# Kernel tuning notes

Hardware: AMD Instinct MI355X
Metric: run time of the kernel (lower is better)

The kernel has to match this reference:

```python
import jax, jax.numpy as jnp
import numpy as np

EMBED = 768
HEADS = 12
HEAD = EMBED // HEADS  # 64
NO_ROPE = 1
GRID = 32
S_IMG = GRID * GRID
SEQ = S_IMG + NO_ROPE
BATCH = 8
SCALE = HEAD ** -0.5


def _rope_tables():
    # VisionRotaryEmbeddingFast(dim=half_head_dim=HEAD//2, pt_seq_len=GRID)
    dim = HEAD // 2  # 32 per spatial axis
    inv_freq = 1.0 / (10000.0 ** (np.arange(0, dim, 2, dtype=np.float32) / dim))  # [dim//2]
    t = np.arange(GRID, dtype=np.float32)
    f = t[:, None] * inv_freq[None, :]              # [GRID, dim//2]
    f = np.repeat(f, 2, axis=-1)                    # interleaved pairs -> [GRID, dim]
    fh = np.broadcast_to(f[:, None, :], (GRID, GRID, dim))
    fw = np.broadcast_to(f[None, :, :], (GRID, GRID, dim))
    freqs = np.concatenate([fh, fw], axis=-1).reshape(S_IMG, HEAD)  # [S_IMG, HEAD]
    return jnp.asarray(np.cos(freqs)), jnp.asarray(np.sin(freqs))

ROPE_COS, ROPE_SIN = _rope_tables()


def _rel_pos_index():
    ch, cw = np.meshgrid(np.arange(GRID), np.arange(GRID), indexing='ij')
    coords = np.stack([ch.ravel(), cw.ravel()])          # [2, S_IMG]
    rel = coords[:, :, None] - coords[:, None, :]        # [2, S_IMG, S_IMG]
    rel = rel.transpose(1, 2, 0).astype(np.int64)
    rel[:, :, 0] += GRID - 1
    rel[:, :, 1] += GRID - 1
    rel[:, :, 0] *= 2 * GRID - 1
    return jnp.asarray(rel.sum(-1))                      # [S_IMG, S_IMG]

REL_INDEX = _rel_pos_index()


def _rotate_half(x):
    # pairs are interleaved: (d r) with r=2
    x2 = x.reshape(*x.shape[:-1], -1, 2)
    return jnp.stack([-x2[..., 1], x2[..., 0]], axis=-1).reshape(x.shape)


def _apply_rope(t):
    # t: [B, H, S, HEAD]; first NO_ROPE tokens bypass rope
    t_cls, t_img = t[:, :, :NO_ROPE, :], t[:, :, NO_ROPE:, :]
    t_img = t_img * ROPE_COS + _rotate_half(t_img) * ROPE_SIN
    return jnp.concatenate([t_cls, t_img], axis=2)


def setup_inputs() -> dict:
    key = jax.random.key(0)
    ks = jax.random.split(key, 6)
    std = EMBED ** -0.5
    return {
        'x': jax.random.normal(ks[0], (BATCH, SEQ, EMBED), jnp.float32),
        'qkv_w': jax.random.normal(ks[1], (3 * EMBED, EMBED), jnp.float32) * std,
        'qkv_b': jnp.zeros((3 * EMBED,), jnp.float32),
        'proj_w': jax.random.normal(ks[2], (EMBED, EMBED), jnp.float32) * std,
        'proj_b': jnp.zeros((EMBED,), jnp.float32),
        'rel_bias_table': jax.random.normal(ks[3], ((2 * GRID - 1) * (2 * GRID - 1), HEADS), jnp.float32) * 0.02,
        'key_padding_mask': jnp.zeros((BATCH, SEQ), jnp.bool_),
    }


def reference(x, qkv_w, qkv_b, proj_w, proj_b, rel_bias_table, key_padding_mask):
    B, S, _ = x.shape
    qkv = x @ qkv_w.T + qkv_b                                  # [B,S,3E]
    qkv = qkv.reshape(B, S, 3, HEADS, HEAD).transpose(2, 0, 3, 1, 4)
    q, k, v = qkv[0], qkv[1], qkv[2]                            # [B,H,S,D]
    q = _apply_rope(q)
    k = _apply_rope(k)
    scores = jnp.einsum('bhqd,bhkd->bhqk', q, k) * SCALE        # [B,H,S,S]
    # relative position bias on image-token sub-block
    bias = rel_bias_table[REL_INDEX]                            # [S_IMG,S_IMG,H]
    bias = bias.transpose(2, 0, 1)                              # [H,S_IMG,S_IMG]
    scores = scores.at[:, :, NO_ROPE:, NO_ROPE:].add(bias[None])
    neg = jnp.finfo(scores.dtype).min
    scores = jnp.where(key_padding_mask[:, None, None, :], neg, scores)
    attn = jax.nn.softmax(scores, axis=-1)
    ctx = jnp.einsum('bhqk,bhkd->bhqd', attn, v)
    ctx = ctx.transpose(0, 2, 1, 3).reshape(B, S, EMBED)
    return ctx @ proj_w.T + proj_b
```

## Files before the change

kernel.cpp:

```cpp
#include <hip/hip_runtime.h>
#include <math.h>

#define EMBED 768
#define NHEADS 12
#define HDIM 64
#define SEQ 1025
#define NBATCH 8
#define BHCOUNT (NBATCH*NHEADS)
#define MROWS (NBATCH*SEQ)
#define QKV_N (3*EMBED)
#define QKV_ELEMS (BHCOUNT*SEQ*HDIM)
#define BT_N 3969
#define MASKPAD 1088
#define QMUL 0.1803368801111204f
#define LOG2E 1.4426950408889634f
#define NX4 1574400
#define NW4 442368
#define NP4 147456

typedef __attribute__((ext_vector_type(8))) short bf16x8;
typedef __attribute__((ext_vector_type(4))) float f32x4;

static __device__ inline unsigned short f2bf(float f) {
    unsigned u = __float_as_uint(f);
    unsigned r = (u + 0x7FFF + ((u >> 16) & 1)) >> 16;
    return (unsigned short)r;
}

static __device__ inline unsigned int cvtpk(float a, float b) {
    unsigned int r;
    asm("v_cvt_pk_bf16_f32 %0, %1, %2" : "=v"(r) : "v"(a), "v"(b));
    return r;
}

static __device__ inline void gld16(const unsigned short* g, unsigned short* l) {
    __builtin_amdgcn_global_load_lds(
        (const __attribute__((address_space(1))) unsigned int*)g,
        (__attribute__((address_space(3))) unsigned int*)l,
        16, 0, 0);
}

__global__ __launch_bounds__(256)
void f2bf3_kernel(const float* __restrict__ x, const float* __restrict__ w,
                  const float* __restrict__ pw,
                  unsigned short* __restrict__ xbf, unsigned short* __restrict__ wbf,
                  unsigned short* __restrict__ pwbf)
{
    int i = blockIdx.x * 256 + threadIdx.x;
    const float* src; unsigned short* dst; int off;
    if (i < NX4)            { src = x;  dst = xbf;  off = i; }
    else if (i < NX4 + NW4) { src = w;  dst = wbf;  off = i - NX4; }
    else if (i < NX4 + NW4 + NP4) { src = pw; dst = pwbf; off = i - NX4 - NW4; }
    else return;
    float4 v = *reinterpret_cast<const float4*>(&src[off << 2]);
    ushort4 o;
    o.x = f2bf(v.x); o.y = f2bf(v.y); o.z = f2bf(v.z); o.w = f2bf(v.w);
    *reinterpret_cast<ushort4*>(&dst[off << 2]) = o;
}

__global__ __launch_bounds__(256)
void setup_tables_kernel(const float* __restrict__ bt, float* __restrict__ btT,
                         const unsigned char* __restrict__ m, unsigned char* __restrict__ mp,
                         float* __restrict__ cosT, float* __restrict__ sinT)
{
    const int bid = blockIdx.x, tid = threadIdx.x;
    if (bid < 256) {
        int s = (bid << 2) + (tid >> 6);
        int d = tid & 63;
        int pos = (d < 32) ? (s >> 5) : (s & 31);
        int j = (d & 31) >> 1;
        float ang = (float)pos * expf(-(float)j * 0.5756462732485115f);
        cosT[(s << 6) + d] = cosf(ang);
        sinT[(s << 6) + d] = sinf(ang);
    } else if (bid < 256 + 187) {
        int e = (bid - 256) * 256 + tid;
        if (e < NHEADS * BT_N) {
            int h = e / BT_N, idx = e - h * BT_N;
            btT[h * BT_N + idx] = bt[idx * NHEADS + h] * LOG2E;
        }
    } else {
        int b = bid - 443;
        for (int i = tid; i < MASKPAD; i += 256)
            mp[b * MASKPAD + i] = (i < SEQ) ? m[b * SEQ + i] : (unsigned char)0;
    }
}

__global__ __launch_bounds__(256)
void qkv_mfma_kernel(const unsigned short* __restrict__ xbf,
                     const unsigned short* __restrict__ wbf,
                     const float* __restrict__ bias,
                     const float* __restrict__ cosT, const float* __restrict__ sinT,
                     unsigned short* __restrict__ qout, unsigned short* __restrict__ kout,
                     unsigned short* __restrict__ vout)
{
    __shared__ unsigned short As[128][32];
    __shared__ unsigned short Bs[128][32];
    const int m0 = blockIdx.x * 128;
    const int n0 = blockIdx.y * 128;
    const int tid = threadIdx.x;
    const int w = tid >> 6, lane = tid & 63;
    const int li = lane & 15, lg = lane >> 4;
    const int wr = w >> 1, wc = w & 1;

    f32x4 acc[4][4];
    #pragma unroll
    for (int mi = 0; mi < 4; ++mi)
        #pragma unroll
        for (int nj = 0; nj < 4; ++nj) acc[mi][nj] = (f32x4){0.f, 0.f, 0.f, 0.f};

    for (int kt = 0; kt < 24; ++kt) {
        const int k0 = kt << 5;
        #pragma unroll
        for (int c = 0; c < 2; ++c) {
            const int idx = c * 256 + tid;
            const int row = idx >> 2, slot = idx & 3;
            int grow = m0 + row; if (grow > MROWS - 1) grow = MROWS - 1;
            gld16(&xbf[(long)grow * EMBED + k0 + slot * 8], &As[0][0] + idx * 8);
            gld16(&wbf[(long)(n0 + row) * EMBED + k0 + slot * 8], &Bs[0][0] + idx * 8);
        }
        __syncthreads();

        bf16x8 af[4], bfr[4];
        #pragma unroll
        for (int mi = 0; mi < 4; ++mi)
            af[mi] = *reinterpret_cast<const bf16x8*>(&As[wr * 64 + mi * 16 + li][lg * 8]);
        #pragma unroll
        for (int nj = 0; nj < 4; ++nj)
            bfr[nj] = *reinterpret_cast<const bf16x8*>(&Bs[wc * 64 + nj * 16 + li][lg * 8]);
        __builtin_amdgcn_s_setprio(1);
        #pragma unroll
        for (int mi = 0; mi < 4; ++mi)
            #pragma unroll
            for (int nj = 0; nj < 4; ++nj)
                acc[mi][nj] = __builtin_amdgcn_mfma_f32_16x16x32_bf16(
                    af[mi], bfr[nj], acc[mi][nj], 0, 0, 0);
        __builtin_amdgcn_s_setprio(0);
        __syncthreads();
    }

    int brow[4][4], srow[4][4];
    #pragma unroll
    for (int mi = 0; mi < 4; ++mi)
        #pragma unroll
        for (int r = 0; r < 4; ++r) {
            int m = m0 + wr * 64 + mi * 16 + lg * 4 + r;
            int mm = (m < MROWS) ? m : (MROWS - 1);
            int bb = mm / SEQ;
            brow[mi][r] = bb;
            srow[mi][r] = mm - bb * SEQ;
        }

    #pragma unroll
    for (int nj = 0; nj < 4; ++nj) {
        const int n = n0 + wc * 64 + nj * 16 + li;
        const int which = n / EMBED;
        const int nh = n - which * EMBED;
        const int h = nh >> 6, d = nh & 63;
        unsigned short* outp = (which == 0) ? qout : (which == 1) ? kout : vout;
        const float mul = (which == 0) ? QMUL : 1.0f;
        const float bn = bias[n];
        const bool dorope = which < 2;
        const float sgn = (d & 1) ? 1.f : -1.f;
        #pragma unroll
        for (int mi = 0; mi < 4; ++mi)
            #pragma unroll
            for (int r = 0; r < 4; ++r) {
                const int m = m0 + wr * 64 + mi * 16 + lg * 4 + r;
                float v = acc[mi][nj][r] + bn;
                float pv = __shfl_xor(v, 1, 64);
                if (m < MROWS) {
                    const int bb = brow[mi][r], s = srow[mi][r];
                    if (dorope && s >= 1) {
                        const int p = s - 1;
                        v = v * cosT[(p << 6) + d] + sgn * pv * sinT[(p << 6) + d];
                    }
                    outp[((long)(bb * NHEADS + h) * SEQ + s) * HDIM + d] = f2bf(v * mul);
                }
            }
    }
}

__global__ __launch_bounds__(256)
void attn_mfma_kernel(const unsigned short* __restrict__ qg,
                      const unsigned short* __restrict__ kg,
                      const unsigned short* __restrict__ vg,
                      const float* __restrict__ btT,
                      const unsigned char* __restrict__ maskpad,
                      unsigned short* __restrict__ ctx)
{
    __shared__ unsigned short QPs[64][64];
    __shared__ unsigned short Ks[2][64][64];
    __shared__ unsigned short Vts[2][64][64];

    const int i = (int)blockIdx.x;
    const int xcd = i & 7, jb = i >> 3;
    const int bh = xcd * 12 + (jb % 12);
    const int q0 = (jb / 12) * 64;
    const int b = bh / NHEADS, h = bh % NHEADS;
    const int tid = threadIdx.x;
    const int w = tid >> 6;
    const int lane = tid & 63;
    const int lg = lane >> 4;
    const int li = lane & 15;
    const int qrow = (w << 4) + li;
    const int swzr = (li & 7) << 3;

    const unsigned short* qbase = qg + (long)bh * (SEQ * HDIM);
    const unsigned short* kbase = kg + (long)bh * (SEQ * HDIM);
    const unsigned short* vbase = vg + (long)bh * (SEQ * HDIM);
    const unsigned char* maskp = maskpad + b * MASKPAD;
    const float* btTh = btT + h * BT_N;

    const int sidx0 = tid, sidx1 = 256 + tid;
    const int sr0 = sidx0 >> 3, sc0 = (sidx0 & 7) << 3;
    const int sr1 = sidx1 >> 3, sc1 = (sidx1 & 7) << 3;

    {
        int qi0 = q0 + sr0; if (qi0 > SEQ - 1) qi0 = SEQ - 1;
        int qi1 = q0 + sr1; if (qi1 > SEQ - 1) qi1 = SEQ - 1;
        gld16(&qbase[(long)qi0 * HDIM + (sc0 ^ ((sr0 & 7) << 3))], &QPs[0][0] + sidx0 * 8);
        gld16(&qbase[(long)qi1 * HDIM + (sc1 ^ ((sr1 & 7) << 3))], &QPs[0][0] + sidx1 * 8);
        gld16(&kbase[(long)sr0 * HDIM + (sc0 ^ ((sr0 & 7) << 3))], &Ks[0][0][0] + sidx0 * 8);
        gld16(&kbase[(long)sr1 * HDIM + (sc1 ^ ((sr1 & 7) << 3))], &Ks[0][0][0] + sidx1 * 8);
    }
    int4 vreg[2];
    vreg[0] = *reinterpret_cast<const int4*>(&vbase[(long)sr0 * HDIM + sc0]);
    vreg[1] = *reinterpret_cast<const int4*>(&vbase[(long)sr1 * HDIM + sc1]);
    __syncthreads();

    bf16x8 qf[2];
    #pragma unroll
    for (int dk = 0; dk < 2; ++dk)
        qf[dk] = *reinterpret_cast<const bf16x8*>(&QPs[qrow][(dk * 32 + (lg << 3)) ^ swzr]);

    const int qi_l = q0 + qrow;
    const float bq = (qi_l >= 1) ? 1.0f : 0.0f;
    int qp = qi_l - 1; if (qp < 0) qp = 0; if (qp > 1023) qp = 1023;
    const int qcode = (qp >> 5) * 63 + (qp & 31) + 1984;

    {
        union { int4 v; unsigned short u[8]; } t0, t1;
        t0.v = vreg[0]; t1.v = vreg[1];
        const int cb30 = sc0 >> 3, cb31 = sc1 >> 3;
        #pragma unroll
        for (int e = 0; e < 8; ++e) {
            Vts[0][sc0 + e][sr0 ^ (((e ^ cb30) & 7) << 3)] = t0.u[e];
            Vts[0][sc1 + e][sr1 ^ (((e ^ cb31) & 7) << 3)] = t1.u[e];
        }
    }
    __syncthreads();

    float m_l = -1e30f, l_l = 0.f;
    f32x4 acco[4];
    #pragma unroll
    for (int j = 0; j < 4; ++j) acco[j] = (f32x4){0.f, 0.f, 0.f, 0.f};

    int kc[4][4];
    for (int kt = 0; kt < 17; ++kt) {
        const int k0 = kt * 64;
        const int cur = kt & 1;

        if (kt < 16) {
            const int k0n = k0 + 64;
            vreg[0] = (k0n + sr0 < SEQ)
                ? *reinterpret_cast<const int4*>(&vbase[(long)(k0n + sr0) * HDIM + sc0])
                : make_int4(0, 0, 0, 0);
            vreg[1] = (k0n + sr1 < SEQ)
                ? *reinterpret_cast<const int4*>(&vbase[(long)(k0n + sr1) * HDIM + sc1])
                : make_int4(0, 0, 0, 0);
            int ki0 = k0n + sr0; if (ki0 > SEQ - 1) ki0 = SEQ - 1;
            int ki1 = k0n + sr1; if (ki1 > SEQ - 1) ki1 = SEQ - 1;
            gld16(&kbase[(long)ki0 * HDIM + (sc0 ^ ((sr0 & 7) << 3))],
                  &Ks[cur ^ 1][0][0] + sidx0 * 8);
            gld16(&kbase[(long)ki1 * HDIM + (sc1 ^ ((sr1 & 7) << 3))],
                  &Ks[cur ^ 1][0][0] + sidx1 * 8);
        }

        unsigned int b4[4];
        if (kt >= 1 && kt <= 15) {
            #pragma unroll
            for (int j = 0; j < 4; ++j) {
                b4[j] = *reinterpret_cast<const unsigned int*>(&maskp[k0 + (j << 4) + (lg << 2)]);
                #pragma unroll
                for (int r = 0; r < 4; ++r) kc[j][r] += 126;
            }
        } else {
            #pragma unroll
            for (int j = 0; j < 4; ++j) {
                unsigned int bb = 0;
                #pragma unroll
                for (int r = 0; r < 4; ++r) {
                    const int ki = k0 + (j << 4) + (lg << 2) + r;
                    unsigned int dead = (ki >= SEQ) ? 1u : (unsigned int)maskp[ki];
                    bb |= (dead ? 1u : 0u) << (r * 8);
                    int kp = ki - 1; if (kp < 0) kp = 0; if (kp > 1023) kp = 1023;
                    kc[j][r] = (kp >> 5) * 63 + (kp & 31);
                }
                b4[j] = bb;
            }
        }
        float bv[4][4];
        #pragma unroll
        for (int j = 0; j < 4; ++j)
            #pragma unroll
            for (int r = 0; r < 4; ++r)
                bv[j][r] = btTh[qcode - kc[j][r]];

        f32x4 accs[4];
        #pragma unroll
        for (int j = 0; j < 4; ++j) accs[j] = (f32x4){0.f, 0.f, 0.f, 0.f};
        __builtin_amdgcn_s_setprio(1);
        #pragma unroll
        for (int dk = 0; dk < 2; ++dk) {
            const int cb = dk * 32 + (lg << 3);
            #pragma unroll
            for (int j = 0; j < 4; ++j) {
                bf16x8 kf = *reinterpret_cast<const bf16x8*>(&Ks[cur][(j << 4) + li][cb ^ swzr]);
                accs[j] = __builtin_amdgcn_mfma_f32_16x16x32_bf16(kf, qf[dk], accs[j], 0, 0, 0);
            }
        }
        __builtin_amdgcn_s_setprio(0);

        float sv[4][4];
        #pragma unroll
        for (int j = 0; j < 4; ++j)
            #pragma unroll
            for (int r = 0; r < 4; ++r)
                sv[j][r] = accs[j][r] + bv[j][r] * bq;
        if (kt == 0 && lg == 0)
            sv[0][0] = accs[0][0];
        if (__any((b4[0] | b4[1] | b4[2] | b4[3]) != 0)) {
            #pragma unroll
            for (int j = 0; j < 4; ++j)
                #pragma unroll
                for (int r = 0; r < 4; ++r)
                    if ((b4[j] >> (r * 8)) & 0xFF) sv[j][r] = -1e30f;
        }

        float mj[4];
        #pragma unroll
        for (int j = 0; j < 4; ++j)
            mj[j] = fmaxf(fmaxf(sv[j][0], sv[j][1]), fmaxf(sv[j][2], sv[j][3]));
        float mx = fmaxf(fmaxf(mj[0], mj[1]), fmaxf(mj[2], mj[3]));
        mx = fmaxf(mx, __shfl_xor(mx, 16, 64));
        mx = fmaxf(mx, __shfl_xor(mx, 32, 64));
        if (__any(mx > m_l + 8.0f)) {
            const float mnew = fmaxf(m_l, mx);
            const float alpha = __builtin_amdgcn_exp2f(m_l - mnew);
            float al[4];
            #pragma unroll
            for (int r = 0; r < 4; ++r) al[r] = __shfl(alpha, (lg << 2) + r, 64);
            #pragma unroll
            for (int j = 0; j < 4; ++j)
                #pragma unroll
                for (int r = 0; r < 4; ++r) acco[j][r] *= al[r];
            l_l *= alpha;
            m_l = mnew;
        }
        float rs = 0.f;
        #pragma unroll
        for (int j = 0; j < 4; ++j) {
            float p0 = __builtin_amdgcn_exp2f(sv[j][0] - m_l);
            float p1 = __builtin_amdgcn_exp2f(sv[j][1] - m_l);
            float p2 = __builtin_amdgcn_exp2f(sv[j][2] - m_l);
            float p3 = __builtin_amdgcn_exp2f(sv[j][3] - m_l);
            rs += (p0 + p1) + (p2 + p3);
            *reinterpret_cast<uint2*>(&QPs[qrow][((j << 4) + (lg << 2)) ^ swzr]) =
                make_uint2(cvtpk(p0, p1), cvtpk(p2, p3));
        }
        rs += __shfl_xor(rs, 16, 64);
        rs += __shfl_xor(rs, 32, 64);
        l_l += rs;

        __builtin_amdgcn_s_setprio(1);
        #pragma unroll
        for (int kk = 0; kk < 2; ++kk) {
            const int cb = kk * 32 + (lg << 3);
            bf16x8 pf = *reinterpret_cast<const bf16x8*>(&QPs[qrow][cb ^ swzr]);
            #pragma unroll
            for (int j = 0; j < 4; ++j) {
                const int drow = (j << 4) + li;
                const int sv2 = ((drow ^ (drow >> 3)) & 7) << 3;
                bf16x8 vf = *reinterpret_cast<const bf16x8*>(&Vts[cur][drow][cb ^ sv2]);
                acco[j] = __builtin_amdgcn_mfma_f32_16x16x32_bf16(pf, vf, acco[j], 0, 0, 0);
            }
        }
        __builtin_amdgcn_s_setprio(0);

        if (kt < 16) {
            union { int4 v; unsigned short u[8]; } t0, t1;
            t0.v = vreg[0]; t1.v = vreg[1];
            const int cb30 = sc0 >> 3, cb31 = sc1 >> 3;
            #pragma unroll
            for (int e = 0; e < 8; ++e) {
                Vts[cur ^ 1][sc0 + e][sr0 ^ (((e ^ cb30) & 7) << 3)] = t0.u[e];
                Vts[cur ^ 1][sc1 + e][sr1 ^ (((e ^ cb31) & 7) << 3)] = t1.u[e];
            }
            __syncthreads();
        }
    }

    float lb[4];
    #pragma unroll
    for (int r = 0; r < 4; ++r) lb[r] = __shfl(l_l, (lg << 2) + r, 64);
    #pragma unroll
    for (int r = 0; r < 4; ++r) {
        const int rl = (lg << 2) + r;
        const int qi = q0 + (w << 4) + rl;
        if (qi < SEQ) {
            const float inv = 1.0f / lb[r];
            #pragma unroll
            for (int j = 0; j < 4; ++j)
                ctx[(long)(b * SEQ + qi) * EMBED + h * HDIM + (j << 4) + li] =
                    f2bf(acco[j][r] * inv);
        }
    }
}

__global__ __launch_bounds__(256)
void proj_mfma_kernel(const unsigned short* __restrict__ ctxbf,
                      const unsigned short* __restrict__ pwbf,
                      const float* __restrict__ bias, float* __restrict__ out)
{
    __shared__ unsigned short As[128][32];
    __shared__ unsigned short Bs[128][32];
    const int m0 = blockIdx.x * 128;
    const int n0 = blockIdx.y * 128;
    const int tid = threadIdx.x;
    const int w = tid >> 6, lane = tid & 63;
    const int li = lane & 15, lg = lane >> 4;
    const int wr = w >> 1, wc = w & 1;

    f32x4 acc[4][4];
    #pragma unroll
    for (int mi = 0; mi < 4; ++mi)
        #pragma unroll
        for (int nj = 0; nj < 4; ++nj) acc[mi][nj] = (f32x4){0.f, 0.f, 0.f, 0.f};

    for (int kt = 0; kt < 24; ++kt) {
        const int k0 = kt << 5;
        #pragma unroll
        for (int c = 0; c < 2; ++c) {
            const int idx = c * 256 + tid;
            const int row = idx >> 2, slot = idx & 3;
            int grow = m0 + row; if (grow > MROWS - 1) grow = MROWS - 1;
            gld16(&ctxbf[(long)grow * EMBED + k0 + slot * 8], &As[0][0] + idx * 8);
            gld16(&pwbf[(long)(n0 + row) * EMBED + k0 + slot * 8], &Bs[0][0] + idx * 8);
        }
        __syncthreads();

        bf16x8 af[4], bfr[4];
        #pragma unroll
        for (int mi = 0; mi < 4; ++mi)
            af[mi] = *reinterpret_cast<const bf16x8*>(&As[wr * 64 + mi * 16 + li][lg * 8]);
        #pragma unroll
        for (int nj = 0; nj < 4; ++nj)
            bfr[nj] = *reinterpret_cast<const bf16x8*>(&Bs[wc * 64 + nj * 16 + li][lg * 8]);
        __builtin_amdgcn_s_setprio(1);
        #pragma unroll
        for (int mi = 0; mi < 4; ++mi)
            #pragma unroll
            for (int nj = 0; nj < 4; ++nj)
                acc[mi][nj] = __builtin_amdgcn_mfma_f32_16x16x32_bf16(
                    af[mi], bfr[nj], acc[mi][nj], 0, 0, 0);
        __builtin_amdgcn_s_setprio(0);
        __syncthreads();
    }

    #pragma unroll
    for (int nj = 0; nj < 4; ++nj) {
        const int n = n0 + wc * 64 + nj * 16 + li;
        const float bn = bias[n];
        #pragma unroll
        for (int mi = 0; mi < 4; ++mi)
            #pragma unroll
            for (int r = 0; r < 4; ++r) {
                const int m = m0 + wr * 64 + mi * 16 + lg * 4 + r;
                if (m < MROWS)
                    out[(long)m * EMBED + n] = acc[mi][nj][r] + bn;
            }
    }
}

extern "C" void kernel_launch(void* const* d_in, const int* in_sizes, int n_in,
                              void* d_out, int out_size, void* d_ws, size_t ws_size,
                              hipStream_t stream) {
    const float* x       = (const float*)d_in[0];
    const float* qkv_w   = (const float*)d_in[1];
    const float* qkv_b   = (const float*)d_in[2];
    const float* proj_w  = (const float*)d_in[3];
    const float* proj_b  = (const float*)d_in[4];
    const float* rel_bt  = (const float*)d_in[5];
    const unsigned char* kmask = (const unsigned char*)d_in[6];
    float* out = (float*)d_out;

    unsigned short* qbuf  = (unsigned short*)d_ws;
    unsigned short* kbuf  = qbuf + QKV_ELEMS;
    unsigned short* vbuf  = kbuf + QKV_ELEMS;
    unsigned short* ctxbf = vbuf + QKV_ELEMS;
    unsigned short* xbf   = ctxbf + QKV_ELEMS;
    unsigned short* wbf   = xbf + QKV_ELEMS;
    unsigned short* pwbf  = wbf + QKV_N * EMBED;
    float* cosT = (float*)(pwbf + EMBED * EMBED);
    float* sinT = cosT + 1024 * HDIM;
    float* btT  = sinT + 1024 * HDIM;
    unsigned char* maskpad = (unsigned char*)(btT + NHEADS * BT_N);

    const int ntot4 = NX4 + NW4 + NP4;
    f2bf3_kernel<<<(ntot4 + 255) / 256, 256, 0, stream>>>(x, qkv_w, proj_w, xbf, wbf, pwbf);
    setup_tables_kernel<<<256 + 187 + NBATCH, 256, 0, stream>>>(
        rel_bt, btT, kmask, maskpad, cosT, sinT);

    qkv_mfma_kernel<<<dim3((MROWS + 127) / 128, QKV_N / 128), 256, 0, stream>>>(
        xbf, wbf, qkv_b, cosT, sinT, qbuf, kbuf, vbuf);
    attn_mfma_kernel<<<17 * BHCOUNT, 256, 0, stream>>>(
        qbuf, kbuf, vbuf, btT, maskpad, ctxbf);
    proj_mfma_kernel<<<dim3((MROWS + 127) / 128, EMBED / 128), 256, 0, stream>>>(
        ctxbf, pwbf, proj_b, out);
}
```

Measured before the change: 244.5 us.

## Enlarge attention query tile to 128 rows with 512-thread blocks

The attention kernel now processes 128 query rows per block with eight waves instead of 64 rows with four, so each K/V tile loaded into shared memory serves twice as many queries. The grid shrinks from 17 to 9 query blocks per batch-head, and each thread now loads one K and one V chunk per iteration instead of two. This halves K/V global traffic per query and the per-thread staging work. In exchange the grid has fewer, larger blocks, the last tile is more heavily padded (1025 rows split into 128-row tiles), and register pressure under the 512-thread launch bound may lower occupancy.

```diff
diff --git a/kernel.cpp b/kernel.cpp
--- a/kernel.cpp
+++ b/kernel.cpp
@@ -180,7 +180,7 @@
     }
 }
 
-__global__ __launch_bounds__(256)
+__global__ __launch_bounds__(512)
 void attn_mfma_kernel(const unsigned short* __restrict__ qg,
                       const unsigned short* __restrict__ kg,
                       const unsigned short* __restrict__ vg,
@@ -188,14 +188,14 @@
                       const unsigned char* __restrict__ maskpad,
                       unsigned short* __restrict__ ctx)
 {
-    __shared__ unsigned short QPs[64][64];
+    __shared__ unsigned short QPs[128][64];
     __shared__ unsigned short Ks[2][64][64];
     __shared__ unsigned short Vts[2][64][64];
 
     const int i = (int)blockIdx.x;
     const int xcd = i & 7, jb = i >> 3;
     const int bh = xcd * 12 + (jb % 12);
-    const int q0 = (jb / 12) * 64;
+    const int q0 = (jb / 12) * 128;
     const int b = bh / NHEADS, h = bh % NHEADS;
     const int tid = threadIdx.x;
     const int w = tid >> 6;
@@ -211,21 +211,19 @@
     const unsigned char* maskp = maskpad + b * MASKPAD;
     const float* btTh = btT + h * BT_N;
 
-    const int sidx0 = tid, sidx1 = 256 + tid;
-    const int sr0 = sidx0 >> 3, sc0 = (sidx0 & 7) << 3;
-    const int sr1 = sidx1 >> 3, sc1 = (sidx1 & 7) << 3;
+    const int sr = tid >> 3, sc = (tid & 7) << 3;
 
     {
-        int qi0 = q0 + sr0; if (qi0 > SEQ - 1) qi0 = SEQ - 1;
-        int qi1 = q0 + sr1; if (qi1 > SEQ - 1) qi1 = SEQ - 1;
-        gld16(&qbase[(long)qi0 * HDIM + (sc0 ^ ((sr0 & 7) << 3))], &QPs[0][0] + sidx0 * 8);
-        gld16(&qbase[(long)qi1 * HDIM + (sc1 ^ ((sr1 & 7) << 3))], &QPs[0][0] + sidx1 * 8);
-        gld16(&kbase[(long)sr0 * HDIM + (sc0 ^ ((sr0 & 7) << 3))], &Ks[0][0][0] + sidx0 * 8);
-        gld16(&kbase[(long)sr1 * HDIM + (sc1 ^ ((sr1 & 7) << 3))], &Ks[0][0][0] + sidx1 * 8);
-    }
-    int4 vreg[2];
-    vreg[0] = *reinterpret_cast<const int4*>(&vbase[(long)sr0 * HDIM + sc0]);
-    vreg[1] = *reinterpret_cast<const int4*>(&vbase[(long)sr1 * HDIM + sc1]);
+        const int idx0 = tid, idx1 = 512 + tid;
+        const int r0 = idx0 >> 3, c0 = (idx0 & 7) << 3;
+        const int r1 = idx1 >> 3, c1 = (idx1 & 7) << 3;
+        int qi0 = q0 + r0; if (qi0 > SEQ - 1) qi0 = SEQ - 1;
+        int qi1 = q0 + r1; if (qi1 > SEQ - 1) qi1 = SEQ - 1;
+        gld16(&qbase[(long)qi0 * HDIM + (c0 ^ ((r0 & 7) << 3))], &QPs[0][0] + idx0 * 8);
+        gld16(&qbase[(long)qi1 * HDIM + (c1 ^ ((r1 & 7) << 3))], &QPs[0][0] + idx1 * 8);
+        gld16(&kbase[(long)sr * HDIM + (sc ^ ((sr & 7) << 3))], &Ks[0][0][0] + tid * 8);
+    }
+    int4 vreg = *reinterpret_cast<const int4*>(&vbase[(long)sr * HDIM + sc]);
     __syncthreads();
 
     bf16x8 qf[2];
@@ -239,14 +237,11 @@
     const int qcode = (qp >> 5) * 63 + (qp & 31) + 1984;
 
     {
-        union { int4 v; unsigned short u[8]; } t0, t1;
-        t0.v = vreg[0]; t1.v = vreg[1];
-        const int cb30 = sc0 >> 3, cb31 = sc1 >> 3;
-        #pragma unroll
-        for (int e = 0; e < 8; ++e) {
-            Vts[0][sc0 + e][sr0 ^ (((e ^ cb30) & 7) << 3)] = t0.u[e];
-            Vts[0][sc1 + e][sr1 ^ (((e ^ cb31) & 7) << 3)] = t1.u[e];
-        }
+        union { int4 v; unsigned short u[8]; } t0; t0.v = vreg;
+        const int cb3 = sc >> 3;
+        #pragma unroll
+        for (int e = 0; e < 8; ++e)
+            Vts[0][sc + e][sr ^ (((e ^ cb3) & 7) << 3)] = t0.u[e];
     }
     __syncthreads();
 
@@ -262,18 +257,12 @@
 
         if (kt < 16) {
             const int k0n = k0 + 64;
-            vreg[0] = (k0n + sr0 < SEQ)
-                ? *reinterpret_cast<const int4*>(&vbase[(long)(k0n + sr0) * HDIM + sc0])
+            vreg = (k0n + sr < SEQ)
+                ? *reinterpret_cast<const int4*>(&vbase[(long)(k0n + sr) * HDIM + sc])
                 : make_int4(0, 0, 0, 0);
-            vreg[1] = (k0n + sr1 < SEQ)
-                ? *reinterpret_cast<const int4*>(&vbase[(long)(k0n + sr1) * HDIM + sc1])
-                : make_int4(0, 0, 0, 0);
-            int ki0 = k0n + sr0; if (ki0 > SEQ - 1) ki0 = SEQ - 1;
-            int ki1 = k0n + sr1; if (ki1 > SEQ - 1) ki1 = SEQ - 1;
-            gld16(&kbase[(long)ki0 * HDIM + (sc0 ^ ((sr0 & 7) << 3))],
-                  &Ks[cur ^ 1][0][0] + sidx0 * 8);
-            gld16(&kbase[(long)ki1 * HDIM + (sc1 ^ ((sr1 & 7) << 3))],
-                  &Ks[cur ^ 1][0][0] + sidx1 * 8);
+            int ki0 = k0n + sr; if (ki0 > SEQ - 1) ki0 = SEQ - 1;
+            gld16(&kbase[(long)ki0 * HDIM + (sc ^ ((sr & 7) << 3))],
+                  &Ks[cur ^ 1][0][0] + tid * 8);
         }
 
         unsigned int b4[4];
@@ -388,14 +377,11 @@
         __builtin_amdgcn_s_setprio(0);
 
         if (kt < 16) {
-            union { int4 v; unsigned short u[8]; } t0, t1;
-            t0.v = vreg[0]; t1.v = vreg[1];
-            const int cb30 = sc0 >> 3, cb31 = sc1 >> 3;
-            #pragma unroll
-            for (int e = 0; e < 8; ++e) {
-                Vts[cur ^ 1][sc0 + e][sr0 ^ (((e ^ cb30) & 7) << 3)] = t0.u[e];
-                Vts[cur ^ 1][sc1 + e][sr1 ^ (((e ^ cb31) & 7) << 3)] = t1.u[e];
-            }
+            union { int4 v; unsigned short u[8]; } t0; t0.v = vreg;
+            const int cb3 = sc >> 3;
+            #pragma unroll
+            for (int e = 0; e < 8; ++e)
+                Vts[cur ^ 1][sc + e][sr ^ (((e ^ cb3) & 7) << 3)] = t0.u[e];
             __syncthreads();
         }
     }
@@ -513,7 +499,7 @@
 
     qkv_mfma_kernel<<<dim3((MROWS + 127) / 128, QKV_N / 128), 256, 0, stream>>>(
         xbf, wbf, qkv_b, cosT, sinT, qbuf, kbuf, vbuf);
-    attn_mfma_kernel<<<17 * BHCOUNT, 256, 0, stream>>>(
+    attn_mfma_kernel<<<9 * BHCOUNT, 512, 0, stream>>>(
         qbuf, kbuf, vbuf, btT, maskpad, ctxbf);
     proj_mfma_kernel<<<dim3((MROWS + 127) / 128, EMBED / 128), 256, 0, stream>>>(
         ctxbf, pwbf, proj_b, out);
```

Measured after the change: 257.1 us. 5.1% more time.

## Switch attention to 32x32 MFMA with 128-row query tiles and register-resident P

Applied to the files above, without the earlier changes.

Rewrites the attention kernel to use 32x32x16 bf16 MFMA, with each wave owning 32 query rows, so a block covers 128 queries and the grid shrinks from 17 to 9 tiles per head. The softmax probabilities stay in registers and are rearranged with v_permlane32_swap instead of going through shared memory, which removes the QPs buffer and its LDS round trip. Q is loaded straight from global into registers, and relative-bias values are fetched as float4 vector loads. The aim is to cut LDS traffic and to halve K/V reloads per query row. The cost is higher register pressure and fewer blocks, which may lower occupancy.

```diff
diff --git a/kernel.cpp b/kernel.cpp
--- a/kernel.cpp
+++ b/kernel.cpp
@@ -20,6 +20,8 @@
 
 typedef __attribute__((ext_vector_type(8))) short bf16x8;
 typedef __attribute__((ext_vector_type(4))) float f32x4;
+typedef __attribute__((ext_vector_type(16))) float f32x16;
+typedef __attribute__((ext_vector_type(4))) unsigned int u32x4;
 
 static __device__ inline unsigned short f2bf(float f) {
     unsigned u = __float_as_uint(f);
@@ -188,22 +190,19 @@
                       const unsigned char* __restrict__ maskpad,
                       unsigned short* __restrict__ ctx)
 {
-    __shared__ unsigned short QPs[64][64];
     __shared__ unsigned short Ks[2][64][64];
     __shared__ unsigned short Vts[2][64][64];
 
     const int i = (int)blockIdx.x;
     const int xcd = i & 7, jb = i >> 3;
     const int bh = xcd * 12 + (jb % 12);
-    const int q0 = (jb / 12) * 64;
+    const int q0 = (jb / 12) * 128;
     const int b = bh / NHEADS, h = bh % NHEADS;
     const int tid = threadIdx.x;
     const int w = tid >> 6;
     const int lane = tid & 63;
-    const int lg = lane >> 4;
-    const int li = lane & 15;
-    const int qrow = (w << 4) + li;
-    const int swzr = (li & 7) << 3;
+    const int l31 = lane & 31;
+    const int hi = lane >> 5;
 
     const unsigned short* qbase = qg + (long)bh * (SEQ * HDIM);
     const unsigned short* kbase = kg + (long)bh * (SEQ * HDIM);
@@ -214,30 +213,28 @@
     const int sidx0 = tid, sidx1 = 256 + tid;
     const int sr0 = sidx0 >> 3, sc0 = (sidx0 & 7) << 3;
     const int sr1 = sidx1 >> 3, sc1 = (sidx1 & 7) << 3;
-
-    {
-        int qi0 = q0 + sr0; if (qi0 > SEQ - 1) qi0 = SEQ - 1;
-        int qi1 = q0 + sr1; if (qi1 > SEQ - 1) qi1 = SEQ - 1;
-        gld16(&qbase[(long)qi0 * HDIM + (sc0 ^ ((sr0 & 7) << 3))], &QPs[0][0] + sidx0 * 8);
-        gld16(&qbase[(long)qi1 * HDIM + (sc1 ^ ((sr1 & 7) << 3))], &QPs[0][0] + sidx1 * 8);
-        gld16(&kbase[(long)sr0 * HDIM + (sc0 ^ ((sr0 & 7) << 3))], &Ks[0][0][0] + sidx0 * 8);
-        gld16(&kbase[(long)sr1 * HDIM + (sc1 ^ ((sr1 & 7) << 3))], &Ks[0][0][0] + sidx1 * 8);
-    }
+    const int kswz0 = ((sr0 ^ (sr0 >> 3)) & 7) << 3;
+    const int kswz1 = ((sr1 ^ (sr1 >> 3)) & 7) << 3;
+
+    gld16(&kbase[(long)sr0 * HDIM + (sc0 ^ kswz0)], &Ks[0][0][0] + sidx0 * 8);
+    gld16(&kbase[(long)sr1 * HDIM + (sc1 ^ kswz1)], &Ks[0][0][0] + sidx1 * 8);
     int4 vreg[2];
     vreg[0] = *reinterpret_cast<const int4*>(&vbase[(long)sr0 * HDIM + sc0]);
     vreg[1] = *reinterpret_cast<const int4*>(&vbase[(long)sr1 * HDIM + sc1]);
-    __syncthreads();
-
-    bf16x8 qf[2];
-    #pragma unroll
-    for (int dk = 0; dk < 2; ++dk)
-        qf[dk] = *reinterpret_cast<const bf16x8*>(&QPs[qrow][(dk * 32 + (lg << 3)) ^ swzr]);
-
+
+    const int qrow = (w << 5) + l31;
     const int qi_l = q0 + qrow;
+    const int qiq = (qi_l > SEQ - 1) ? (SEQ - 1) : qi_l;
+    bf16x8 qf[4];
+    #pragma unroll
+    for (int s = 0; s < 4; ++s)
+        qf[s] = *reinterpret_cast<const bf16x8*>(&qbase[(long)qiq * HDIM + s * 16 + hi * 8]);
+
     const float bq = (qi_l >= 1) ? 1.0f : 0.0f;
     int qp = qi_l - 1; if (qp < 0) qp = 0; if (qp > 1023) qp = 1023;
     const int qcode = (qp >> 5) * 63 + (qp & 31) + 1984;
 
+    __syncthreads();
     {
         union { int4 v; unsigned short u[8]; } t0, t1;
         t0.v = vreg[0]; t1.v = vreg[1];
@@ -251,11 +248,11 @@
     __syncthreads();
 
     float m_l = -1e30f, l_l = 0.f;
-    f32x4 acco[4];
-    #pragma unroll
-    for (int j = 0; j < 4; ++j) acco[j] = (f32x4){0.f, 0.f, 0.f, 0.f};
-
-    int kc[4][4];
+    f32x16 acco[2];
+    #pragma unroll
+    for (int r = 0; r < 16; ++r) { acco[0][r] = 0.f; acco[1][r] = 0.f; }
+
+    int kcb[2][4];
     for (int kt = 0; kt < 17; ++kt) {
         const int k0 = kt * 64;
         const int cur = kt & 1;
@@ -270,119 +267,150 @@
                 : make_int4(0, 0, 0, 0);
             int ki0 = k0n + sr0; if (ki0 > SEQ - 1) ki0 = SEQ - 1;
             int ki1 = k0n + sr1; if (ki1 > SEQ - 1) ki1 = SEQ - 1;
-            gld16(&kbase[(long)ki0 * HDIM + (sc0 ^ ((sr0 & 7) << 3))],
-                  &Ks[cur ^ 1][0][0] + sidx0 * 8);
-            gld16(&kbase[(long)ki1 * HDIM + (sc1 ^ ((sr1 & 7) << 3))],
-                  &Ks[cur ^ 1][0][0] + sidx1 * 8);
-        }
-
-        unsigned int b4[4];
+            gld16(&kbase[(long)ki0 * HDIM + (sc0 ^ kswz0)], &Ks[cur ^ 1][0][0] + sidx0 * 8);
+            gld16(&kbase[(long)ki1 * HDIM + (sc1 ^ kswz1)], &Ks[cur ^ 1][0][0] + sidx1 * 8);
+        }
+
+        unsigned int b4[2][4];
+        float bvf[2][16];
         if (kt >= 1 && kt <= 15) {
             #pragma unroll
-            for (int j = 0; j < 4; ++j) {
-                b4[j] = *reinterpret_cast<const unsigned int*>(&maskp[k0 + (j << 4) + (lg << 2)]);
+            for (int j = 0; j < 2; ++j)
                 #pragma unroll
-                for (int r = 0; r < 4; ++r) kc[j][r] += 126;
-            }
+                for (int t = 0; t < 4; ++t) {
+                    b4[j][t] = *reinterpret_cast<const unsigned int*>(
+                        &maskp[k0 + j * 32 + t * 8 + hi * 4]);
+                    kcb[j][t] += 126;
+                    const int base = qcode - kcb[j][t];
+                    if (t == 0 && hi == 0) {
+                        float4 f = *reinterpret_cast<const float4*>(&btTh[base - 34]);
+                        bvf[j][0] = btTh[base]; bvf[j][1] = f.z;
+                        bvf[j][2] = f.y;        bvf[j][3] = f.x;
+                    } else {
+                        float4 f = *reinterpret_cast<const float4*>(&btTh[base - 3]);
+                        bvf[j][t * 4 + 0] = f.w; bvf[j][t * 4 + 1] = f.z;
+                        bvf[j][t * 4 + 2] = f.y; bvf[j][t * 4 + 3] = f.x;
+                    }
+                }
         } else {
             #pragma unroll
-            for (int j = 0; j < 4; ++j) {
-                unsigned int bb = 0;
+            for (int j = 0; j < 2; ++j)
                 #pragma unroll
-                for (int r = 0; r < 4; ++r) {
-                    const int ki = k0 + (j << 4) + (lg << 2) + r;
-                    unsigned int dead = (ki >= SEQ) ? 1u : (unsigned int)maskp[ki];
-                    bb |= (dead ? 1u : 0u) << (r * 8);
-                    int kp = ki - 1; if (kp < 0) kp = 0; if (kp > 1023) kp = 1023;
-                    kc[j][r] = (kp >> 5) * 63 + (kp & 31);
+                for (int t = 0; t < 4; ++t) {
+                    unsigned int bb = 0;
+                    #pragma unroll
+                    for (int ri = 0; ri < 4; ++ri) {
+                        const int ki = k0 + j * 32 + t * 8 + hi * 4 + ri;
+                        const int kic = (ki > SEQ - 1) ? (SEQ - 1) : ki;
+                        unsigned int dead = (ki >= SEQ) ? 1u : (unsigned int)maskp[kic];
+                        bb |= (dead ? 1u : 0u) << (ri * 8);
+                        int kp = ki - 1; if (kp < 0) kp = 0; if (kp > 1023) kp = 1023;
+                        const int kcv = (kp >> 5) * 63 + (kp & 31);
+                        bvf[j][t * 4 + ri] = btTh[qcode - kcv];
+                    }
+                    b4[j][t] = bb;
+                    if (kt == 0) {
+                        const int kp0 = j * 32 + t * 8 + hi * 4 - 1;
+                        kcb[j][t] = (kp0 >> 5) * 63 + (kp0 & 31);
+                    }
                 }
-                b4[j] = bb;
-            }
-        }
-        float bv[4][4];
-        #pragma unroll
-        for (int j = 0; j < 4; ++j)
-            #pragma unroll
-            for (int r = 0; r < 4; ++r)
-                bv[j][r] = btTh[qcode - kc[j][r]];
-
-        f32x4 accs[4];
-        #pragma unroll
-        for (int j = 0; j < 4; ++j) accs[j] = (f32x4){0.f, 0.f, 0.f, 0.f};
+        }
+
+        f32x16 accs[2];
+        #pragma unroll
+        for (int r = 0; r < 16; ++r) { accs[0][r] = 0.f; accs[1][r] = 0.f; }
         __builtin_amdgcn_s_setprio(1);
         #pragma unroll
-        for (int dk = 0; dk < 2; ++dk) {
-            const int cb = dk * 32 + (lg << 3);
-            #pragma unroll
-            for (int j = 0; j < 4; ++j) {
-                bf16x8 kf = *reinterpret_cast<const bf16x8*>(&Ks[cur][(j << 4) + li][cb ^ swzr]);
-                accs[j] = __builtin_amdgcn_mfma_f32_16x16x32_bf16(kf, qf[dk], accs[j], 0, 0, 0);
+        for (int j = 0; j < 2; ++j) {
+            const int rswz = ((l31 ^ (j * 4 + (l31 >> 3))) & 7) << 3;
+            const unsigned short* krow = &Ks[cur][j * 32 + l31][0];
+            #pragma unroll
+            for (int s = 0; s < 4; ++s) {
+                bf16x8 kf = *reinterpret_cast<const bf16x8*>(&krow[(s * 16 + hi * 8) ^ rswz]);
+                accs[j] = __builtin_amdgcn_mfma_f32_32x32x16_bf16(kf, qf[s], accs[j], 0, 0, 0);
             }
         }
         __builtin_amdgcn_s_setprio(0);
 
-        float sv[4][4];
-        #pragma unroll
-        for (int j = 0; j < 4; ++j)
-            #pragma unroll
-            for (int r = 0; r < 4; ++r)
-                sv[j][r] = accs[j][r] + bv[j][r] * bq;
-        if (kt == 0 && lg == 0)
-            sv[0][0] = accs[0][0];
-        if (__any((b4[0] | b4[1] | b4[2] | b4[3]) != 0)) {
-            #pragma unroll
-            for (int j = 0; j < 4; ++j)
+        const float bq00 = (kt == 0 && hi == 0) ? 0.0f : bq;
+        accs[0][0] += bvf[0][0] * bq00;
+        #pragma unroll
+        for (int j = 0; j < 2; ++j)
+            #pragma unroll
+            for (int r = 0; r < 16; ++r)
+                if (!(j == 0 && r == 0))
+                    accs[j][r] += bvf[j][r] * bq;
+        if (__any((b4[0][0] | b4[0][1] | b4[0][2] | b4[0][3] |
+                   b4[1][0] | b4[1][1] | b4[1][2] | b4[1][3]) != 0)) {
+            #pragma unroll
+            for (int j = 0; j < 2; ++j)
                 #pragma unroll
-                for (int r = 0; r < 4; ++r)
-                    if ((b4[j] >> (r * 8)) & 0xFF) sv[j][r] = -1e30f;
-        }
-
-        float mj[4];
-        #pragma unroll
-        for (int j = 0; j < 4; ++j)
-            mj[j] = fmaxf(fmaxf(sv[j][0], sv[j][1]), fmaxf(sv[j][2], sv[j][3]));
-        float mx = fmaxf(fmaxf(mj[0], mj[1]), fmaxf(mj[2], mj[3]));
-        mx = fmaxf(mx, __shfl_xor(mx, 16, 64));
+                for (int r = 0; r < 16; ++r)
+                    if ((b4[j][r >> 2] >> ((r & 3) * 8)) & 0xFF) accs[j][r] = -1e30f;
+        }
+
+        float mx = accs[0][0];
+        #pragma unroll
+        for (int j = 0; j < 2; ++j)
+            #pragma unroll
+            for (int r = 0; r < 16; ++r) mx = fmaxf(mx, accs[j][r]);
         mx = fmaxf(mx, __shfl_xor(mx, 32, 64));
         if (__any(mx > m_l + 8.0f)) {
             const float mnew = fmaxf(m_l, mx);
             const float alpha = __builtin_amdgcn_exp2f(m_l - mnew);
-            float al[4];
-            #pragma unroll
-            for (int r = 0; r < 4; ++r) al[r] = __shfl(alpha, (lg << 2) + r, 64);
-            #pragma unroll
-            for (int j = 0; j < 4; ++j)
-                #pragma unroll
-                for (int r = 0; r < 4; ++r) acco[j][r] *= al[r];
+            #pragma unroll
+            for (int r = 0; r < 16; ++r) {
+                const float al = __shfl(alpha, (r & 3) + 8 * (r >> 2) + 4 * hi, 64);
+                acco[0][r] *= al;
+                acco[1][r] *= al;
+            }
             l_l *= alpha;
             m_l = mnew;
         }
         float rs = 0.f;
         #pragma unroll
-        for (int j = 0; j < 4; ++j) {
-            float p0 = __builtin_amdgcn_exp2f(sv[j][0] - m_l);
-            float p1 = __builtin_amdgcn_exp2f(sv[j][1] - m_l);
-            float p2 = __builtin_amdgcn_exp2f(sv[j][2] - m_l);
-            float p3 = __builtin_amdgcn_exp2f(sv[j][3] - m_l);
-            rs += (p0 + p1) + (p2 + p3);
-            *reinterpret_cast<uint2*>(&QPs[qrow][((j << 4) + (lg << 2)) ^ swzr]) =
-                make_uint2(cvtpk(p0, p1), cvtpk(p2, p3));
-        }
-        rs += __shfl_xor(rs, 16, 64);
+        for (int j = 0; j < 2; ++j)
+            #pragma unroll
+            for (int r = 0; r < 16; ++r) {
+                accs[j][r] = __builtin_amdgcn_exp2f(accs[j][r] - m_l);
+                rs += accs[j][r];
+            }
         rs += __shfl_xor(rs, 32, 64);
         l_l += rs;
 
+        unsigned int W[2][8];
+        #pragma unroll
+        for (int j = 0; j < 2; ++j)
+            #pragma unroll
+            for (int p = 0; p < 8; ++p)
+                W[j][p] = cvtpk(accs[j][2 * p], accs[j][2 * p + 1]);
+        #pragma unroll
+        for (int j = 0; j < 2; ++j)
+            #pragma unroll
+            for (int sg = 0; sg < 2; ++sg) {
+                unsigned int a0 = W[j][4 * sg + 0], a2 = W[j][4 * sg + 2];
+                asm volatile("v_permlane32_swap_b32 %0, %1" : "+v"(a0), "+v"(a2));
+                W[j][4 * sg + 0] = a0; W[j][4 * sg + 2] = a2;
+                unsigned int a1 = W[j][4 * sg + 1], a3 = W[j][4 * sg + 3];
+                asm volatile("v_permlane32_swap_b32 %0, %1" : "+v"(a1), "+v"(a3));
+                W[j][4 * sg + 1] = a1; W[j][4 * sg + 3] = a3;
+            }
+
         __builtin_amdgcn_s_setprio(1);
         #pragma unroll
-        for (int kk = 0; kk < 2; ++kk) {
-            const int cb = kk * 32 + (lg << 3);
-            bf16x8 pf = *reinterpret_cast<const bf16x8*>(&QPs[qrow][cb ^ swzr]);
-            #pragma unroll
-            for (int j = 0; j < 4; ++j) {
-                const int drow = (j << 4) + li;
-                const int sv2 = ((drow ^ (drow >> 3)) & 7) << 3;
-                bf16x8 vf = *reinterpret_cast<const bf16x8*>(&Vts[cur][drow][cb ^ sv2]);
-                acco[j] = __builtin_amdgcn_mfma_f32_16x16x32_bf16(pf, vf, acco[j], 0, 0, 0);
+        for (int j2 = 0; j2 < 2; ++j2) {
+            const int vswz = ((l31 ^ (j2 * 4 + (l31 >> 3))) & 7) << 3;
+            const unsigned short* vrow = &Vts[cur][j2 * 32 + l31][0];
+            #pragma unroll
+            for (int s = 0; s < 4; ++s) {
+                bf16x8 vf = *reinterpret_cast<const bf16x8*>(&vrow[(s * 16 + hi * 8) ^ vswz]);
+                u32x4 aw;
+                aw[0] = W[s >> 1][4 * (s & 1) + 0];
+                aw[1] = W[s >> 1][4 * (s & 1) + 1];
+                aw[2] = W[s >> 1][4 * (s & 1) + 2];
+                aw[3] = W[s >> 1][4 * (s & 1) + 3];
+                bf16x8 pa = __builtin_bit_cast(bf16x8, aw);
+                acco[j2] = __builtin_amdgcn_mfma_f32_32x32x16_bf16(pa, vf, acco[j2], 0, 0, 0);
             }
         }
         __builtin_amdgcn_s_setprio(0);
@@ -400,19 +428,15 @@
         }
     }
 
-    float lb[4];
-    #pragma unroll
-    for (int r = 0; r < 4; ++r) lb[r] = __shfl(l_l, (lg << 2) + r, 64);
-    #pragma unroll
-    for (int r = 0; r < 4; ++r) {
-        const int rl = (lg << 2) + r;
-        const int qi = q0 + (w << 4) + rl;
+    #pragma unroll
+    for (int r = 0; r < 16; ++r) {
+        const int ql = (r & 3) + 8 * (r >> 2) + 4 * hi;
+        const float lb = __shfl(l_l, ql, 64);
+        const int qi = q0 + (w << 5) + ql;
         if (qi < SEQ) {
-            const float inv = 1.0f / lb[r];
-            #pragma unroll
-            for (int j = 0; j < 4; ++j)
-                ctx[(long)(b * SEQ + qi) * EMBED + h * HDIM + (j << 4) + li] =
-                    f2bf(acco[j][r] * inv);
+            const float inv = 1.0f / lb;
+            ctx[(long)(b * SEQ + qi) * EMBED + h * HDIM + l31] = f2bf(acco[0][r] * inv);
+            ctx[(long)(b * SEQ + qi) * EMBED + h * HDIM + 32 + l31] = f2bf(acco[1][r] * inv);
         }
     }
 }
@@ -513,7 +537,7 @@
 
     qkv_mfma_kernel<<<dim3((MROWS + 127) / 128, QKV_N / 128), 256, 0, stream>>>(
         xbf, wbf, qkv_b, cosT, sinT, qbuf, kbuf, vbuf);
-    attn_mfma_kernel<<<17 * BHCOUNT, 256, 0, stream>>>(
+    attn_mfma_kernel<<<9 * BHCOUNT, 256, 0, stream>>>(
         qbuf, kbuf, vbuf, btT, maskpad, ctxbf);
     proj_mfma_kernel<<<dim3((MROWS + 127) / 128, EMBED / 128), 256, 0, stream>>>(
         ctxbf, pwbf, proj_b, out);
```

After: 225.1 us. 7.9% less time.
